# Kernel optimization log

Hardware: AMD Instinct MI355X
Metric: run time of the kernel (lower is better)

## Reference

```python
import jax, jax.numpy as jnp
import numpy as np

N_NODES = 50000
N_GRAPHS = 64


def gcn_layer(x, W, b, src, dst, norm, n):
    # PyG GCNConv: h = x @ W; aggregate norm-weighted messages at dst; add bias
    h = x @ W
    msg = h[src] * norm[:, None]          # [E_tot, out_dim] gather
    out = jax.ops.segment_sum(msg, dst, num_segments=n)
    return out + b


def to_dense_batch(x, batch, max_num, num_graphs):
    n = x.shape[0]
    counts = jax.ops.segment_sum(jnp.ones((n,), x.dtype), batch, num_segments=num_graphs)
    starts = jnp.concatenate([jnp.zeros((1,), jnp.int32),
                              jnp.cumsum(counts.astype(jnp.int32))[:-1]])
    pos = jnp.arange(n, dtype=jnp.int32) - starts[batch]
    valid = pos < max_num
    b_idx = jnp.where(valid, batch, num_graphs)   # overflow -> dummy row
    p_idx = jnp.where(valid, pos, 0)
    dense = jnp.zeros((num_graphs + 1, max_num, x.shape[1]), x.dtype)
    dense = dense.at[b_idx, p_idx].set(x)
    return dense[:num_graphs]


def setup_inputs() -> dict:
    key = jax.random.key(0)
    ks = jax.random.split(key, 12)
    F0, F2, F3, OUT = 54, 108, 216, 200
    x = jax.random.normal(ks[0], (N_NODES, F0), jnp.float32)
    edge_index = jax.random.randint(ks[1], (2, 800000), 0, N_NODES, jnp.int64)
    batch = jnp.sort(jax.random.randint(ks[2], (N_NODES,), 0, N_GRAPHS, jnp.int64))
    def glorot(k, shp):
        lim = 1.0 / np.sqrt(shp[0])
        return jax.random.uniform(k, shp, jnp.float32, -lim, lim)
    return {
        "x": x, "edge_index": edge_index, "batch": batch, "max_num": 1000,
        "W1": glorot(ks[3], (F0, F0)), "b1": jnp.zeros((F0,), jnp.float32),
        "W2": glorot(ks[4], (F0, F2)), "b2": jnp.zeros((F2,), jnp.float32),
        "W3": glorot(ks[5], (F2, F3)), "b3": jnp.zeros((F3,), jnp.float32),
        "Wf": glorot(ks[6], (F3, OUT)), "bf": glorot(ks[7], (OUT,)),
    }


def reference(x, edge_index, batch, max_num, W1, b1, W2, b2, W3, b3, Wf, bf):
    n = x.shape[0]
    loops = jnp.arange(n, dtype=edge_index.dtype)
    src = jnp.concatenate([edge_index[0], loops])
    dst = jnp.concatenate([edge_index[1], loops])
    # symmetric GCN normalization with self-loops (edge_weight = 1)
    deg = jax.ops.segment_sum(jnp.ones_like(dst, jnp.float32), dst, num_segments=n)
    dinv = jax.lax.rsqrt(deg)  # deg >= 1 due to self-loops
    norm = dinv[src] * dinv[dst]

    h = jax.nn.relu(gcn_layer(x, W1, b1, src, dst, norm, n))
    h = jax.nn.relu(gcn_layer(h, W2, b2, src, dst, norm, n))
    h = jax.nn.relu(gcn_layer(h, W3, b3, src, dst, norm, n))
    h = h @ Wf + bf
    return to_dense_batch(h, batch, max_num, N_GRAPHS)
```

## Files before the change

kernel.cpp:

```cpp
#include <hip/hip_runtime.h>
#include <hip/hip_bf16.h>

#define N_GRAPHS 64

typedef __bf16 bf16x8 __attribute__((ext_vector_type(8)));
typedef float floatx4 __attribute__((ext_vector_type(4)));
typedef unsigned short ushort8v __attribute__((ext_vector_type(8)));

__device__ __forceinline__ float b2f(unsigned short u) {
    union { unsigned int i; float f; } v;
    v.i = ((unsigned int)u) << 16;
    return v.f;
}
__device__ __forceinline__ unsigned short f2b(float f) {
    __hip_bfloat16 h = __float2bfloat16(f);
    return *(unsigned short*)&h;
}


__global__ void k_deg(const int* __restrict__ dst, int* __restrict__ deg, int E) {
    int e = blockIdx.x * blockDim.x + threadIdx.x;
    if (e < E) atomicAdd(&deg[dst[e]], 1);
}

__global__ void k_scan_blocks(const int* __restrict__ deg, int* __restrict__ row_start,
                              int* __restrict__ blk_sums, int N) {
    __shared__ int s[256];
    int t = threadIdx.x;
    int i = blockIdx.x * 256 + t;
    int v = (i < N) ? deg[i] : 0;
    s[t] = v;
    __syncthreads();
    for (int off = 1; off < 256; off <<= 1) {
        int x = (t >= off) ? s[t - off] : 0;
        __syncthreads();
        s[t] += x;
        __syncthreads();
    }
    if (i < N) row_start[i] = s[t] - v;
    if (t == 255) blk_sums[blockIdx.x] = s[255];
}

__global__ void k_scan_tot(const int* __restrict__ blk_sums, int nb, int* __restrict__ blk_off) {
    __shared__ int s[256];
    int t = threadIdx.x;
    int v = (t < nb) ? blk_sums[t] : 0;
    s[t] = v;
    __syncthreads();
    for (int off = 1; off < 256; off <<= 1) {
        int x = (t >= off) ? s[t - off] : 0;
        __syncthreads();
        s[t] += x;
        __syncthreads();
    }
    if (t < nb) blk_off[t] = s[t] - v;
}

__global__ void k_scan_add(int* __restrict__ row_start, const int* __restrict__ blk_off,
                           int* __restrict__ cursor, const int* __restrict__ deg,
                           float* __restrict__ dinv, const int* __restrict__ batch,
                           int* __restrict__ gstarts, int N, int E) {
    int i = blockIdx.x * 256 + threadIdx.x;
    if (i < N) {
        int r = row_start[i] + blk_off[blockIdx.x];
        row_start[i] = r;
        cursor[i] = r;
        dinv[i] = 1.0f / sqrtf((float)(deg[i] + 1));
        int b = batch[i];
        int prev = (i == 0) ? -1 : batch[i - 1];
        for (int g = prev + 1; g <= b; ++g) gstarts[g] = i;
        if (i == N - 1)
            for (int g = b + 1; g <= N_GRAPHS; ++g) gstarts[g] = N;
    }
    if (i == 0) row_start[N] = E;
}

__global__ void k_fill(const int* __restrict__ src, const int* __restrict__ dst,
                       int* __restrict__ cursor, int2* __restrict__ col2,
                       const float* __restrict__ dinv, int E) {
    int e = blockIdx.x * blockDim.x + threadIdx.x;
    if (e < E) {
        int s = src[e];
        int p = atomicAdd(&cursor[dst[e]], 1);
        col2[p] = make_int2(s, __float_as_int(dinv[s]));
    }
}

__device__ __forceinline__ void swz_one(const float* __restrict__ W,
                                        unsigned short* __restrict__ Wsw, int i, int K, int Nn,
                                        int KS) {
    int j = i & 7, lane = (i >> 3) & 63;
    int ks = (i >> 9) % KS, nt = i / (512 * KS);
    int n = nt * 16 + (lane & 15);
    int k = ks * 32 + (lane >> 4) * 8 + j;
    float v = (k < K && n < Nn) ? W[(size_t)k * Nn + n] : 0.f;
    Wsw[i] = f2b(v);
}

#define T_W1 (4 * 2 * 512)
#define T_W2 (8 * 2 * 512)
#define T_W3 (14 * 4 * 512)
#define T_WF (13 * 7 * 512)

__global__ void k_prep(const float* __restrict__ W1, const float* __restrict__ W2,
                       const float* __restrict__ W3, const float* __restrict__ Wf,
                       unsigned short* __restrict__ W1s, unsigned short* __restrict__ W2s,
                       unsigned short* __restrict__ W3s, unsigned short* __restrict__ Wfs,
                       const float* __restrict__ x, unsigned short* __restrict__ xb, int Nn) {
    int i = blockIdx.x * 256 + threadIdx.x;
    if (i < T_W1) swz_one(W1, W1s, i, 54, 54, 2);
    else if (i < T_W1 + T_W2) swz_one(W2, W2s, i - T_W1, 54, 108, 2);
    else if (i < T_W1 + T_W2 + T_W3) swz_one(W3, W3s, i - T_W1 - T_W2, 108, 216, 4);
    else if (i < T_W1 + T_W2 + T_W3 + T_WF)
        swz_one(Wf, Wfs, i - T_W1 - T_W2 - T_W3, 216, 200, 7);
    else {
        int ii = i - (T_W1 + T_W2 + T_W3 + T_WF);
        if (ii < Nn * 64) {
            int n = ii >> 6, c = ii & 63;
            xb[ii] = (c < 54) ? f2b(x[(size_t)n * 54 + c]) : (unsigned short)0;
        }
    }
}


template <int P, int AS>
__device__ __forceinline__ void gatherP(const unsigned short* __restrict__ in,
                                        const int* __restrict__ row_start,
                                        const int2* __restrict__ col2,
                                        const float* __restrict__ dinv,
                                        unsigned short* agg_s, int node0, int N, int t) {
    constexpr int S = P / 8;
    constexpr int G = 32 / S;
    int grp = t >> 5, lane5 = t & 31;
    int j = lane5 / S, cl = lane5 % S;
    int rs_a[4], re_a[4];
    float dn_a[4];
#pragma unroll
    for (int rr = 0; rr < 4; ++rr) {
        int n = node0 + grp + rr * 8;
        bool valid = n < N;
        rs_a[rr] = valid ? row_start[n] : 0;
        re_a[rr] = valid ? row_start[n + 1] : 0;
        dn_a[rr] = valid ? dinv[n] : 0.f;
    }
#pragma unroll
    for (int rr = 0; rr < 4; ++rr) {
        int r = grp + rr * 8;
        int n = node0 + r;
        float a[8] = {0.f, 0.f, 0.f, 0.f, 0.f, 0.f, 0.f, 0.f};
        if (n < N) {
            float dn = dn_a[rr];
            if (j == 0) {
                ushort8v u = *((const ushort8v*)(in + (size_t)n * P) + cl);
#pragma unroll
                for (int i = 0; i < 8; ++i) a[i] = dn * b2f(u[i]);
            }
            int re = re_a[rr];
            int e = rs_a[rr] + j;
            for (; e < re; e += 4 * G) {
                int e1 = min(e + G, re - 1);
                int e2 = min(e + 2 * G, re - 1);
                int e3 = min(e + 3 * G, re - 1);
                int2 c0 = col2[e];
                int2 c1 = col2[e1];
                int2 c2 = col2[e2];
                int2 c3 = col2[e3];
                ushort8v v0 = *((const ushort8v*)(in + (size_t)c0.x * P) + cl);
                ushort8v v1 = *((const ushort8v*)(in + (size_t)c1.x * P) + cl);
                ushort8v v2 = *((const ushort8v*)(in + (size_t)c2.x * P) + cl);
                ushort8v v3 = *((const ushort8v*)(in + (size_t)c3.x * P) + cl);
                float d0 = __int_as_float(c0.y);
                float d1 = (e + G < re) ? __int_as_float(c1.y) : 0.f;
                float d2 = (e + 2 * G < re) ? __int_as_float(c2.y) : 0.f;
                float d3 = (e + 3 * G < re) ? __int_as_float(c3.y) : 0.f;
#pragma unroll
                for (int i = 0; i < 8; ++i) {
                    a[i] += d0 * b2f(v0[i]) + d1 * b2f(v1[i]);
                    a[i] += d2 * b2f(v2[i]) + d3 * b2f(v3[i]);
                }
            }
#pragma unroll
            for (int i = 0; i < 8; ++i) a[i] *= dn;
        }
#pragma unroll
        for (int mask = S; mask < 32; mask <<= 1)
#pragma unroll
            for (int i = 0; i < 8; ++i) a[i] += __shfl_xor(a[i], mask, 32);
        if (j == 0) {
            ushort8v rv;
#pragma unroll
            for (int i = 0; i < 8; ++i) rv[i] = f2b(a[i]);
            *((ushort8v*)(agg_s + r * AS) + cl) = rv;
        }
    }
}


template <int P, int FOUT, int FP, int KS, int NT>
__global__ __launch_bounds__(256) void k_layer(
    const unsigned short* __restrict__ in, const int* __restrict__ row_start,
    const int2* __restrict__ col2, const float* __restrict__ dinv,
    const unsigned short* __restrict__ Wsw, const float* __restrict__ bias,
    unsigned short* __restrict__ hout, int N) {
    constexpr int AS = KS * 32 + 8;
    __shared__ __align__(16) unsigned short agg_s[32 * AS];
    int node0 = blockIdx.x * 32;
    int t = threadIdx.x;
    gatherP<P, AS>(in, row_start, col2, dinv, agg_s, node0, N, t);
    __syncthreads();
    int lane = t & 63, wv = t >> 6, m = lane & 15, q = lane >> 4;
    bf16x8 a[2][KS];
#pragma unroll
    for (int mt = 0; mt < 2; ++mt)
#pragma unroll
        for (int ks = 0; ks < KS; ++ks)
            a[mt][ks] = *(const bf16x8*)(agg_s + (mt * 16 + m) * AS + ks * 32 + q * 8);
    for (int nt = wv; nt < NT; nt += 4) {
        const unsigned short* bp = Wsw + ((size_t)(nt * KS) * 64 + lane) * 8;
        bf16x8 bfr[KS];
#pragma unroll
        for (int ks = 0; ks < KS; ++ks) bfr[ks] = *(const bf16x8*)(bp + ks * 512);
        int fo = nt * 16 + m;
        float bb = (fo < FOUT) ? bias[fo] : 0.f;
#pragma unroll
        for (int mt = 0; mt < 2; ++mt) {
            floatx4 c = {0.f, 0.f, 0.f, 0.f};
#pragma unroll
            for (int ks = 0; ks < KS; ++ks)
                c = __builtin_amdgcn_mfma_f32_16x16x32_bf16(a[mt][ks], bfr[ks], c, 0, 0, 0);
#pragma unroll
            for (int r = 0; r < 4; ++r) {
                int n = node0 + mt * 16 + q * 4 + r;
                if (n < N) hout[(size_t)n * FP + fo] = f2b(fmaxf(c[r] + bb, 0.f));
            }
        }
    }
}


__global__ __launch_bounds__(256) void k_l3f(
    const unsigned short* __restrict__ h2, const int* __restrict__ row_start,
    const int2* __restrict__ col2, const float* __restrict__ dinv,
    const unsigned short* __restrict__ W3s, const float* __restrict__ b3,
    const unsigned short* __restrict__ Wfs, const float* __restrict__ bfv,
    const int* __restrict__ batch, const int* __restrict__ gstarts, float* __restrict__ out,
    int N, int mn) {
    constexpr int AS = 136, HS = 232;
    __shared__ __align__(16) unsigned short smem[32 * HS];
    unsigned short* agg_s = smem;
    unsigned short* h3_s = smem;
    int node0 = blockIdx.x * 32;
    int t = threadIdx.x;
    gatherP<128, AS>(h2, row_start, col2, dinv, agg_s, node0, N, t);
    __syncthreads();
    int lane = t & 63, wv = t >> 6, m = lane & 15, q = lane >> 4;
    bf16x8 a1[2][4];
#pragma unroll
    for (int mt = 0; mt < 2; ++mt)
#pragma unroll
        for (int ks = 0; ks < 4; ++ks)
            a1[mt][ks] = *(const bf16x8*)(agg_s + (mt * 16 + m) * AS + ks * 32 + q * 8);
    __syncthreads();
    for (int nt = wv; nt < 14; nt += 4) {
        const unsigned short* bp = W3s + ((size_t)(nt * 4) * 64 + lane) * 8;
        bf16x8 bf0 = *(const bf16x8*)(bp);
        bf16x8 bf1 = *(const bf16x8*)(bp + 512);
        bf16x8 bf2 = *(const bf16x8*)(bp + 1024);
        bf16x8 bf3 = *(const bf16x8*)(bp + 1536);
        int fo = nt * 16 + m;
        float bb = (fo < 216) ? b3[fo] : 0.f;
#pragma unroll
        for (int mt = 0; mt < 2; ++mt) {
            floatx4 c = {0.f, 0.f, 0.f, 0.f};
            c = __builtin_amdgcn_mfma_f32_16x16x32_bf16(a1[mt][0], bf0, c, 0, 0, 0);
            c = __builtin_amdgcn_mfma_f32_16x16x32_bf16(a1[mt][1], bf1, c, 0, 0, 0);
            c = __builtin_amdgcn_mfma_f32_16x16x32_bf16(a1[mt][2], bf2, c, 0, 0, 0);
            c = __builtin_amdgcn_mfma_f32_16x16x32_bf16(a1[mt][3], bf3, c, 0, 0, 0);
#pragma unroll
            for (int r = 0; r < 4; ++r) {
                int row = mt * 16 + q * 4 + r;
                h3_s[row * HS + fo] = f2b(fmaxf(c[r] + bb, 0.f));
            }
        }
    }
    __syncthreads();
    bf16x8 a2[2][7];
#pragma unroll
    for (int mt = 0; mt < 2; ++mt)
#pragma unroll
        for (int ks = 0; ks < 7; ++ks)
            a2[mt][ks] = *(const bf16x8*)(h3_s + (mt * 16 + m) * HS + ks * 32 + q * 8);
    for (int nt = wv; nt < 13; nt += 4) {
        const unsigned short* bp = Wfs + ((size_t)(nt * 7) * 64 + lane) * 8;
        bf16x8 bfr[7];
#pragma unroll
        for (int ks = 0; ks < 7; ++ks) bfr[ks] = *(const bf16x8*)(bp + ks * 512);
        int fo = nt * 16 + m;
        if (fo >= 200) continue;
        float bb = bfv[fo];
#pragma unroll
        for (int mt = 0; mt < 2; ++mt) {
            floatx4 c = {0.f, 0.f, 0.f, 0.f};
#pragma unroll
            for (int ks = 0; ks < 7; ++ks)
                c = __builtin_amdgcn_mfma_f32_16x16x32_bf16(a2[mt][ks], bfr[ks], c, 0, 0, 0);
#pragma unroll
            for (int r = 0; r < 4; ++r) {
                int n = node0 + mt * 16 + q * 4 + r;
                if (n < N) {
                    int b = batch[n];
                    int pos = n - gstarts[b];
                    if (pos >= 0 && pos < mn)
                        out[((size_t)b * mn + pos) * 200 + fo] = c[r] + bb;
                }
            }
        }
    }
}

extern "C" void kernel_launch(void* const* d_in, const int* in_sizes, int n_in,
                              void* d_out, int out_size, void* d_ws, size_t ws_size,
                              hipStream_t stream) {
    const float* x = (const float*)d_in[0];
    const int* ei = (const int*)d_in[1];
    const int* batch = (const int*)d_in[2];
    const float* W1 = (const float*)d_in[4];
    const float* b1 = (const float*)d_in[5];
    const float* W2 = (const float*)d_in[6];
    const float* b2 = (const float*)d_in[7];
    const float* W3 = (const float*)d_in[8];
    const float* b3 = (const float*)d_in[9];
    const float* Wf = (const float*)d_in[10];
    const float* bfv = (const float*)d_in[11];
    float* out = (float*)d_out;

    const int N = in_sizes[2];
    const int E = in_sizes[1] / 2;
    const int mn = out_size / (N_GRAPHS * 200);
    const int* src = ei;
    const int* dst = ei + E;

    char* w = (char*)d_ws;
    auto alloc = [&](size_t bytes) {
        void* p = (void*)w;
        w += (bytes + 255) & ~(size_t)255;
        return p;
    };
    int* deg = (int*)alloc((size_t)N * 4);
    int* row_start = (int*)alloc((size_t)(N + 1) * 4);
    int* blk_sums = (int*)alloc(256 * 4);
    int* blk_off = (int*)alloc(256 * 4);
    int* cursor = (int*)alloc((size_t)N * 4);
    int2* col2 = (int2*)alloc((size_t)E * 8);
    float* dinv = (float*)alloc((size_t)N * 4);
    int* gstarts = (int*)alloc((N_GRAPHS + 1) * 4);
    unsigned short* xb = (unsigned short*)alloc((size_t)N * 64 * 2);
    unsigned short* h1 = (unsigned short*)alloc((size_t)N * 64 * 2);
    unsigned short* h2 = (unsigned short*)alloc((size_t)N * 128 * 2);
    unsigned short* W1s = (unsigned short*)alloc((size_t)T_W1 * 2);
    unsigned short* W2s = (unsigned short*)alloc((size_t)T_W2 * 2);
    unsigned short* W3s = (unsigned short*)alloc((size_t)T_W3 * 2);
    unsigned short* Wfs = (unsigned short*)alloc((size_t)T_WF * 2);
    (void)ws_size;

    hipMemsetAsync(deg, 0, (size_t)N * 4, stream);
    hipMemsetAsync(d_out, 0, (size_t)out_size * sizeof(float), stream);

    int NB = (N + 255) / 256;
    k_deg<<<(E + 255) / 256, 256, 0, stream>>>(dst, deg, E);
    k_scan_blocks<<<NB, 256, 0, stream>>>(deg, row_start, blk_sums, N);
    k_scan_tot<<<1, 256, 0, stream>>>(blk_sums, NB, blk_off);
    k_scan_add<<<NB, 256, 0, stream>>>(row_start, blk_off, cursor, deg, dinv, batch, gstarts,
                                       N, E);
    k_fill<<<(E + 255) / 256, 256, 0, stream>>>(src, dst, cursor, col2, dinv, E);
    int prep_total = T_W1 + T_W2 + T_W3 + T_WF + N * 64;
    k_prep<<<(prep_total + 255) / 256, 256, 0, stream>>>(W1, W2, W3, Wf, W1s, W2s, W3s, Wfs,
                                                         x, xb, N);

    int NBL = (N + 31) / 32;
    k_layer<64, 54, 64, 2, 4><<<NBL, 256, 0, stream>>>(xb, row_start, col2, dinv, W1s, b1,
                                                       h1, N);
    k_layer<64, 108, 128, 2, 8><<<NBL, 256, 0, stream>>>(h1, row_start, col2, dinv, W2s, b2,
                                                         h2, N);
    k_l3f<<<NBL, 256, 0, stream>>>(h2, row_start, col2, dinv, W3s, b3, Wfs, bfv, batch,
                                   gstarts, out, N, mn);
}
```

Before: 309.5 us.

## Stage CSR edge lists in LDS and shrink layer blocks to 16 nodes

The gather now copies each block's contiguous CSR edge range (col, norm) into shared memory with a cooperative load before aggregation, and falls back to global reads when the range exceeds capacity. Self-row features are also prefetched together with the row bounds. The first two layer kernels switch to 16-node, 128-thread blocks with a single MFMA row tile. The goal is to replace scattered per-lane global index loads with coalesced ones and to raise block count and occupancy, at the cost of an extra barrier and more LDS per block.

New measurement: 323.1 us. +4.4%, slower.

```diff
diff --git a/kernel.cpp b/kernel.cpp
--- a/kernel.cpp
+++ b/kernel.cpp
@@ -6,6 +6,8 @@
 typedef __bf16 bf16x8 __attribute__((ext_vector_type(8)));
 typedef float floatx4 __attribute__((ext_vector_type(4)));
 typedef unsigned short ushort8v __attribute__((ext_vector_type(8)));
+
+template <bool B> struct BoolC { static constexpr bool value = B; };
 
 __device__ __forceinline__ float b2f(unsigned short u) {
     union { unsigned int i; float f; } v;
@@ -123,116 +125,139 @@
 }
 
 
-template <int P, int AS>
+template <int P, int AS, int NODES, int NG, int ECAP>
 __device__ __forceinline__ void gatherP(const unsigned short* __restrict__ in,
                                         const int* __restrict__ row_start,
                                         const int2* __restrict__ col2,
                                         const float* __restrict__ dinv,
-                                        unsigned short* agg_s, int node0, int N, int t) {
+                                        unsigned short* agg_s, int2* ecol_s,
+                                        int node0, int N, int t) {
     constexpr int S = P / 8;
     constexpr int G = 32 / S;
+    constexpr int RPG = NODES / NG;
+    constexpr int NTH = NG * 32;
     int grp = t >> 5, lane5 = t & 31;
     int j = lane5 / S, cl = lane5 % S;
-    int rs_a[4], re_a[4];
-    float dn_a[4];
-#pragma unroll
-    for (int rr = 0; rr < 4; ++rr) {
-        int n = node0 + grp + rr * 8;
+    int nlast = node0 + NODES;
+    if (nlast > N) nlast = N;
+    int block_rs = row_start[node0];
+    int block_re = row_start[nlast];
+    int rs_a[RPG], re_a[RPG];
+    float dn_a[RPG];
+    ushort8v self_a[RPG];
+#pragma unroll
+    for (int rr = 0; rr < RPG; ++rr) {
+        int n = node0 + grp + rr * NG;
         bool valid = n < N;
         rs_a[rr] = valid ? row_start[n] : 0;
         re_a[rr] = valid ? row_start[n + 1] : 0;
         dn_a[rr] = valid ? dinv[n] : 0.f;
-    }
-#pragma unroll
-    for (int rr = 0; rr < 4; ++rr) {
-        int r = grp + rr * 8;
-        int n = node0 + r;
-        float a[8] = {0.f, 0.f, 0.f, 0.f, 0.f, 0.f, 0.f, 0.f};
-        if (n < N) {
-            float dn = dn_a[rr];
+        if (valid && j == 0)
+            self_a[rr] = *((const ushort8v*)(in + (size_t)n * P) + cl);
+    }
+    int stage = block_re - block_rs;
+    if (stage > ECAP) stage = ECAP;
+    for (int i = t; i < stage; i += NTH) ecol_s[i] = col2[block_rs + i];
+    __syncthreads();
+
+    auto core = [&](auto staged_c) {
+        constexpr bool ST = decltype(staged_c)::value;
+#pragma unroll
+        for (int rr = 0; rr < RPG; ++rr) {
+            int r = grp + rr * NG;
+            int n = node0 + r;
+            float a[8] = {0.f, 0.f, 0.f, 0.f, 0.f, 0.f, 0.f, 0.f};
+            if (n < N) {
+                float dn = dn_a[rr];
+                if (j == 0) {
+#pragma unroll
+                    for (int i = 0; i < 8; ++i) a[i] = dn * b2f(self_a[rr][i]);
+                }
+                int re = re_a[rr];
+                int e = rs_a[rr] + j;
+                for (; e < re; e += 4 * G) {
+                    int e1 = min(e + G, re - 1);
+                    int e2 = min(e + 2 * G, re - 1);
+                    int e3 = min(e + 3 * G, re - 1);
+                    int2 c0, c1, c2, c3;
+                    if constexpr (ST) {
+                        c0 = ecol_s[e - block_rs];
+                        c1 = ecol_s[e1 - block_rs];
+                        c2 = ecol_s[e2 - block_rs];
+                        c3 = ecol_s[e3 - block_rs];
+                    } else {
+                        c0 = col2[e];
+                        c1 = col2[e1];
+                        c2 = col2[e2];
+                        c3 = col2[e3];
+                    }
+                    ushort8v v0 = *((const ushort8v*)(in + (size_t)c0.x * P) + cl);
+                    ushort8v v1 = *((const ushort8v*)(in + (size_t)c1.x * P) + cl);
+                    ushort8v v2 = *((const ushort8v*)(in + (size_t)c2.x * P) + cl);
+                    ushort8v v3 = *((const ushort8v*)(in + (size_t)c3.x * P) + cl);
+                    float d0 = __int_as_float(c0.y);
+                    float d1 = (e + G < re) ? __int_as_float(c1.y) : 0.f;
+                    float d2 = (e + 2 * G < re) ? __int_as_float(c2.y) : 0.f;
+                    float d3 = (e + 3 * G < re) ? __int_as_float(c3.y) : 0.f;
+#pragma unroll
+                    for (int i = 0; i < 8; ++i) {
+                        a[i] += d0 * b2f(v0[i]) + d1 * b2f(v1[i]);
+                        a[i] += d2 * b2f(v2[i]) + d3 * b2f(v3[i]);
+                    }
+                }
+#pragma unroll
+                for (int i = 0; i < 8; ++i) a[i] *= dn;
+            }
+#pragma unroll
+            for (int mask = S; mask < 32; mask <<= 1)
+#pragma unroll
+                for (int i = 0; i < 8; ++i) a[i] += __shfl_xor(a[i], mask, 32);
             if (j == 0) {
-                ushort8v u = *((const ushort8v*)(in + (size_t)n * P) + cl);
-#pragma unroll
-                for (int i = 0; i < 8; ++i) a[i] = dn * b2f(u[i]);
+                ushort8v rv;
+#pragma unroll
+                for (int i = 0; i < 8; ++i) rv[i] = f2b(a[i]);
+                *((ushort8v*)(agg_s + r * AS) + cl) = rv;
             }
-            int re = re_a[rr];
-            int e = rs_a[rr] + j;
-            for (; e < re; e += 4 * G) {
-                int e1 = min(e + G, re - 1);
-                int e2 = min(e + 2 * G, re - 1);
-                int e3 = min(e + 3 * G, re - 1);
-                int2 c0 = col2[e];
-                int2 c1 = col2[e1];
-                int2 c2 = col2[e2];
-                int2 c3 = col2[e3];
-                ushort8v v0 = *((const ushort8v*)(in + (size_t)c0.x * P) + cl);
-                ushort8v v1 = *((const ushort8v*)(in + (size_t)c1.x * P) + cl);
-                ushort8v v2 = *((const ushort8v*)(in + (size_t)c2.x * P) + cl);
-                ushort8v v3 = *((const ushort8v*)(in + (size_t)c3.x * P) + cl);
-                float d0 = __int_as_float(c0.y);
-                float d1 = (e + G < re) ? __int_as_float(c1.y) : 0.f;
-                float d2 = (e + 2 * G < re) ? __int_as_float(c2.y) : 0.f;
-                float d3 = (e + 3 * G < re) ? __int_as_float(c3.y) : 0.f;
-#pragma unroll
-                for (int i = 0; i < 8; ++i) {
-                    a[i] += d0 * b2f(v0[i]) + d1 * b2f(v1[i]);
-                    a[i] += d2 * b2f(v2[i]) + d3 * b2f(v3[i]);
-                }
-            }
-#pragma unroll
-            for (int i = 0; i < 8; ++i) a[i] *= dn;
         }
-#pragma unroll
-        for (int mask = S; mask < 32; mask <<= 1)
-#pragma unroll
-            for (int i = 0; i < 8; ++i) a[i] += __shfl_xor(a[i], mask, 32);
-        if (j == 0) {
-            ushort8v rv;
-#pragma unroll
-            for (int i = 0; i < 8; ++i) rv[i] = f2b(a[i]);
-            *((ushort8v*)(agg_s + r * AS) + cl) = rv;
-        }
-    }
+    };
+    if (block_re - block_rs <= ECAP) core(BoolC<true>{});
+    else core(BoolC<false>{});
 }
 
 
 template <int P, int FOUT, int FP, int KS, int NT>
-__global__ __launch_bounds__(256) void k_layer(
+__global__ __launch_bounds__(128) void k_layer(
     const unsigned short* __restrict__ in, const int* __restrict__ row_start,
     const int2* __restrict__ col2, const float* __restrict__ dinv,
     const unsigned short* __restrict__ Wsw, const float* __restrict__ bias,
     unsigned short* __restrict__ hout, int N) {
     constexpr int AS = KS * 32 + 8;
-    __shared__ __align__(16) unsigned short agg_s[32 * AS];
-    int node0 = blockIdx.x * 32;
+    __shared__ __align__(16) unsigned short agg_s[16 * AS];
+    __shared__ __align__(16) int2 ecol_s[512];
+    int node0 = blockIdx.x * 16;
     int t = threadIdx.x;
-    gatherP<P, AS>(in, row_start, col2, dinv, agg_s, node0, N, t);
+    gatherP<P, AS, 16, 4, 512>(in, row_start, col2, dinv, agg_s, ecol_s, node0, N, t);
     __syncthreads();
     int lane = t & 63, wv = t >> 6, m = lane & 15, q = lane >> 4;
-    bf16x8 a[2][KS];
-#pragma unroll
-    for (int mt = 0; mt < 2; ++mt)
-#pragma unroll
-        for (int ks = 0; ks < KS; ++ks)
-            a[mt][ks] = *(const bf16x8*)(agg_s + (mt * 16 + m) * AS + ks * 32 + q * 8);
-    for (int nt = wv; nt < NT; nt += 4) {
+    bf16x8 a[KS];
+#pragma unroll
+    for (int ks = 0; ks < KS; ++ks)
+        a[ks] = *(const bf16x8*)(agg_s + m * AS + ks * 32 + q * 8);
+    for (int nt = wv; nt < NT; nt += 2) {
         const unsigned short* bp = Wsw + ((size_t)(nt * KS) * 64 + lane) * 8;
         bf16x8 bfr[KS];
 #pragma unroll
         for (int ks = 0; ks < KS; ++ks) bfr[ks] = *(const bf16x8*)(bp + ks * 512);
         int fo = nt * 16 + m;
         float bb = (fo < FOUT) ? bias[fo] : 0.f;
-#pragma unroll
-        for (int mt = 0; mt < 2; ++mt) {
-            floatx4 c = {0.f, 0.f, 0.f, 0.f};
-#pragma unroll
-            for (int ks = 0; ks < KS; ++ks)
-                c = __builtin_amdgcn_mfma_f32_16x16x32_bf16(a[mt][ks], bfr[ks], c, 0, 0, 0);
-#pragma unroll
-            for (int r = 0; r < 4; ++r) {
-                int n = node0 + mt * 16 + q * 4 + r;
-                if (n < N) hout[(size_t)n * FP + fo] = f2b(fmaxf(c[r] + bb, 0.f));
-            }
+        floatx4 c = {0.f, 0.f, 0.f, 0.f};
+#pragma unroll
+        for (int ks = 0; ks < KS; ++ks)
+            c = __builtin_amdgcn_mfma_f32_16x16x32_bf16(a[ks], bfr[ks], c, 0, 0, 0);
+#pragma unroll
+        for (int r = 0; r < 4; ++r) {
+            int n = node0 + q * 4 + r;
+            if (n < N) hout[(size_t)n * FP + fo] = f2b(fmaxf(c[r] + bb, 0.f));
         }
     }
 }
@@ -247,11 +272,12 @@
     int N, int mn) {
     constexpr int AS = 136, HS = 232;
     __shared__ __align__(16) unsigned short smem[32 * HS];
+    __shared__ __align__(16) int2 ecol_s[1024];
     unsigned short* agg_s = smem;
     unsigned short* h3_s = smem;
     int node0 = blockIdx.x * 32;
     int t = threadIdx.x;
-    gatherP<128, AS>(h2, row_start, col2, dinv, agg_s, node0, N, t);
+    gatherP<128, AS, 32, 8, 1024>(h2, row_start, col2, dinv, agg_s, ecol_s, node0, N, t);
     __syncthreads();
     int lane = t & 63, wv = t >> 6, m = lane & 15, q = lane >> 4;
     bf16x8 a1[2][4];
@@ -377,11 +403,12 @@
     k_prep<<<(prep_total + 255) / 256, 256, 0, stream>>>(W1, W2, W3, Wf, W1s, W2s, W3s, Wfs,
                                                          x, xb, N);
 
-    int NBL = (N + 31) / 32;
-    k_layer<64, 54, 64, 2, 4><<<NBL, 256, 0, stream>>>(xb, row_start, col2, dinv, W1s, b1,
-                                                       h1, N);
-    k_layer<64, 108, 128, 2, 8><<<NBL, 256, 0, stream>>>(h1, row_start, col2, dinv, W2s, b2,
-                                                         h2, N);
-    k_l3f<<<NBL, 256, 0, stream>>>(h2, row_start, col2, dinv, W3s, b3, Wfs, bfv, batch,
-                                   gstarts, out, N, mn);
-}
+    int NBL16 = (N + 15) / 16;
+    k_layer<64, 54, 64, 2, 4><<<NBL16, 128, 0, stream>>>(xb, row_start, col2, dinv, W1s, b1,
+                                                         h1, N);
+    k_layer<64, 108, 128, 2, 8><<<NBL16, 128, 0, stream>>>(h1, row_start, col2, dinv, W2s,
+                                                           b2, h2, N);
+    int NBL32 = (N + 31) / 32;
+    k_l3f<<<NBL32, 256, 0, stream>>>(h2, row_start, col2, dinv, W3s, b3, Wfs, bfv, batch,
+                                     gstarts, out, N, mn);
+}
```
